# Performance work log

Measured on AMD Instinct MI355X. Metric: run time of the kernel, lower is better.

## Reference

```python
import jax, jax.numpy as jnp
import numpy as np
import math

B, S, D_IN, EMBED, H = 4, 1024, 1024, 1024, 16
HD = EMBED // H  # 64


def setup_inputs() -> dict:
    key = jax.random.key(0)
    ks = jax.random.split(key, 8)
    x = jax.random.normal(ks[0], (B, S, D_IN), dtype=jnp.float32)
    mask = jax.random.randint(ks[1], (B, S, S), 0, 2, dtype=jnp.int32)
    weights = jax.random.uniform(ks[2], (B, S, S), dtype=jnp.float32)
    # xavier-uniform-ish scale for projections
    lim_qkv = math.sqrt(6.0 / (D_IN + 3 * EMBED))
    lim_o = math.sqrt(6.0 / (EMBED + EMBED))
    W_qkv = jax.random.uniform(ks[3], (3 * EMBED, D_IN), minval=-lim_qkv, maxval=lim_qkv, dtype=jnp.float32)
    b_qkv = jnp.zeros((3 * EMBED,), dtype=jnp.float32)
    W_o = jax.random.uniform(ks[4], (EMBED, EMBED), minval=-lim_o, maxval=lim_o, dtype=jnp.float32)
    b_o = jnp.zeros((EMBED,), dtype=jnp.float32)
    return {"x": x, "mask": mask, "weights": weights, "W_qkv": W_qkv, "b_qkv": b_qkv, "W_o": W_o, "b_o": b_o}


def reference(x, mask, weights, W_qkv, b_qkv, W_o, b_o):
    b, s, _ = x.shape
    # QKV projection: [b, s, 3*EMBED] -> [b, H, s, 3*HD]
    qkv = (x @ W_qkv.T + b_qkv).reshape(b, s, H, 3 * HD).transpose(0, 2, 1, 3)
    q, k, v = jnp.split(qkv, 3, axis=-1)  # each [b, H, s, HD]
    logits = jnp.einsum('bhqd,bhkd->bhqk', q, k) / math.sqrt(HD)
    logits = jnp.where(mask[:, None, :, :] == 0, jnp.float32(-9e15), logits)
    # weights transposed on last two dims, broadcast over heads
    w = jnp.swapaxes(weights, -2, -1)[:, None, :, :]  # [b, 1, s, s]
    m = jnp.max(logits, axis=-1, keepdims=True)
    e = w * jnp.exp(logits - m)
    attn = e / jnp.sum(e, axis=-1, keepdims=True)
    vals = jnp.einsum('bhqk,bhkd->bhqd', attn, v)
    vals = vals.transpose(0, 2, 1, 3).reshape(b, s, EMBED)
    return vals @ W_o.T + b_o
```

## Files before the change

kernel.cpp:

```cpp
#include <hip/hip_runtime.h>
#include <hip/hip_bf16.h>
#include <stdint.h>

#define SDIM 1024
#define BATCH 4
#define NH 16
#define HDIM 64
#define KDIM 1024
#define N_QKV 3072
#define EMB 1024

typedef uint16_t u16;
typedef __attribute__((ext_vector_type(4))) float f32x4;
typedef __attribute__((ext_vector_type(8))) short bf16x8;
typedef __attribute__((ext_vector_type(8))) unsigned short u16x8;

__device__ __forceinline__ u16 f2bf(float f) {
  union { float f; uint32_t u; } x; x.f = f;
  uint32_t r = x.u + 0x7FFFu + ((x.u >> 16) & 1u);
  return (u16)(r >> 16);
}

__device__ __forceinline__ float bf2f(u16 b) {
  union { uint32_t u; float f; } x; x.u = ((uint32_t)b) << 16;
  return x.f;
}

__device__ __forceinline__ void gload_lds16(const u16* g, u16* l) {
  __builtin_amdgcn_global_load_lds(
      (const __attribute__((address_space(1))) unsigned int*)g,
      (__attribute__((address_space(3))) unsigned int*)l, 16, 0, 0);
}

#define N8_X  524288
#define N8_WQ 393216
#define N8_WO 131072
#define NCVT  1048576
#define NWM3  262144
__global__ void prep_kernel(const float* __restrict__ a, const float* __restrict__ bq,
                            const float* __restrict__ co,
                            u16* __restrict__ oa, u16* __restrict__ ob, u16* __restrict__ oc,
                            const int* __restrict__ mask, const float* __restrict__ wts,
                            u16* __restrict__ wm3) {
  const int total = NCVT + NWM3;
  const size_t SS = (size_t)SDIM * SDIM;
  int stride = gridDim.x * blockDim.x;
  for (int i = blockIdx.x * blockDim.x + threadIdx.x; i < total; i += stride) {
    if (i < NCVT) {
      const float* s; u16* d; int j;
      if (i < N8_X)             { s = a;  d = oa; j = i; }
      else if (i < N8_X + N8_WQ){ s = bq; d = ob; j = i - N8_X; }
      else                      { s = co; d = oc; j = i - N8_X - N8_WQ; }
      const float4* s4 = (const float4*)s + (size_t)j * 2;
      float4 u = s4[0], v = s4[1];
      u16x8 o;
      o[0] = f2bf(u.x); o[1] = f2bf(u.y); o[2] = f2bf(u.z); o[3] = f2bf(u.w);
      o[4] = f2bf(v.x); o[5] = f2bf(v.y); o[6] = f2bf(v.z); o[7] = f2bf(v.w);
      ((u16x8*)d)[j] = o;
    } else {
      int t = i - NCVT;
      int lane = t & 63, kt = (t >> 6) & 15, T = (t >> 10) & 63, b = t >> 16;
      int g2 = lane >> 4, c2 = lane & 15;
      int q = T * 16 + c2;
      const int* mrow = mask + (size_t)b * SS + (size_t)q * SDIM;
      const float* wcol = wts + (size_t)b * SS + q;
      u16* dst = wm3 + ((size_t)(b * 64 + T) * 16 + kt) * 1024 + lane * 16;
      #pragma unroll
      for (int hf = 0; hf < 2; ++hf) {
        int bk = kt * 64 + 8 * g2 + 32 * hf;
        int4 m0 = *(const int4*)(mrow + bk);
        int4 m1 = *(const int4*)(mrow + bk + 4);
        int mm[8] = {m0.x, m0.y, m0.z, m0.w, m1.x, m1.y, m1.z, m1.w};
        u16x8 o;
        #pragma unroll
        for (int e = 0; e < 8; ++e)
          o[e] = mm[e] ? f2bf(wcol[(size_t)(bk + e) * SDIM]) : (u16)0;
        *(u16x8*)(dst + hf * 8) = o;
      }
    }
  }
}

__global__ __launch_bounds__(512, 1) void gemm_qkv(
    const u16* __restrict__ A, const u16* __restrict__ Bm,
    const float* __restrict__ bias,
    u16* __restrict__ Qh, u16* __restrict__ Kh, u16* __restrict__ Vt)
{
  __shared__ char smem[114688];
  const int tid = threadIdx.x;
  const int gid = blockIdx.x;
  const int brow = (gid & 15) * 256, bcol = (gid >> 4) * 192;
  const int wid = tid >> 6, lane = tid & 63;
  const int g = lane >> 4, c = lane & 15, cx = c & 7;
  const int wr = wid & 3, wc = wid >> 2;

  const u16* asrc[4]; int adoff[4];
  #pragma unroll
  for (int j = 0; j < 4; ++j) {
    int i = j * 512 + tid;
    int row = i >> 3, sch = (i & 7) ^ (row & 7);
    asrc[j] = A + (size_t)(brow + row) * KDIM + sch * 8;
    adoff[j] = (j * 512 + wid * 64) * 16;
  }
  const u16* bsrc[3]; int bdoff[3];
  #pragma unroll
  for (int j = 0; j < 3; ++j) {
    int i = j * 512 + tid;
    int row = i >> 3, sch = (i & 7) ^ (row & 7);
    bsrc[j] = Bm + (size_t)(bcol + row) * KDIM + sch * 8;
    bdoff[j] = 32768 + (j * 512 + wid * 64) * 16;
  }

  auto stage = [&](int kt, int slot) {
    char* base = smem + slot * 57344;
    #pragma unroll
    for (int j = 0; j < 4; ++j)
      gload_lds16(asrc[j] + kt * 64, (u16*)(base + adoff[j]));
    #pragma unroll
    for (int j = 0; j < 3; ++j)
      gload_lds16(bsrc[j] + kt * 64, (u16*)(base + bdoff[j]));
  };

  f32x4 acc[4][6] = {};

  stage(0, 0);
  __syncthreads();

  for (int kt = 0; kt < 16; ++kt) {
    if (kt < 15) stage(kt + 1, (kt + 1) & 1);

    const char* As = smem + (kt & 1) * 57344;
    const char* Bs = As + 32768;

    #pragma unroll
    for (int kk = 0; kk < 2; ++kk) {
      bf16x8 af[4], bfr[6];
      #pragma unroll
      for (int m = 0; m < 4; ++m) {
        int row = wr * 64 + m * 16 + c;
        af[m] = *(const bf16x8*)(As + (row << 7) + ((((kk << 2) + g) ^ cx) << 4));
      }
      #pragma unroll
      for (int n = 0; n < 6; ++n) {
        int row = wc * 96 + n * 16 + c;
        bfr[n] = *(const bf16x8*)(Bs + (row << 7) + ((((kk << 2) + g) ^ cx) << 4));
      }
      __builtin_amdgcn_s_setprio(1);
      #pragma unroll
      for (int m = 0; m < 4; ++m)
        #pragma unroll
        for (int n = 0; n < 6; ++n)
          acc[m][n] = __builtin_amdgcn_mfma_f32_16x16x32_bf16(
              af[m], bfr[n], acc[m][n], 0, 0, 0);
      __builtin_amdgcn_s_setprio(0);
    }
    __syncthreads();
  }

  #pragma unroll
  for (int m = 0; m < 4; ++m) {
    #pragma unroll
    for (int n = 0; n < 6; ++n) {
      int col = bcol + wc * 96 + n * 16 + c;
      float bv = bias[col];
      int h = col / 192;
      int rem = col - h * 192;
      int sec = rem >> 6, d = rem & 63;
      #pragma unroll
      for (int r = 0; r < 4; ++r) {
        int row = brow + wr * 64 + m * 16 + g * 4 + r;
        int b = row >> 10, sl = row & 1023;
        float v = acc[m][n][r] + bv;
        if (sec == 0)
          Qh[((size_t)(b * NH + h) * SDIM + sl) * HDIM + d] = f2bf(v * 0.125f);
        else if (sec == 1)
          Kh[((size_t)(b * NH + h) * SDIM + sl) * HDIM + d] = f2bf(v);
        else
          Vt[((size_t)(b * NH + h) * HDIM + d) * SDIM + sl] = f2bf(v);
      }
    }
  }
}

__global__ __launch_bounds__(256) void gemm_bt(
    const u16* __restrict__ A, const u16* __restrict__ Bm,
    const float* __restrict__ bias, float* __restrict__ C,
    int M, int N, int K)
{
  __shared__ u16 As[128 * 64];
  __shared__ u16 Bs[128 * 64];
  const int tid = threadIdx.x;
  const int wid = tid >> 6, lane = tid & 63;
  const int g = lane >> 4, c = lane & 15, cx = c & 7;
  const int wrow = (wid >> 1) * 64, wcol = (wid & 1) * 64;
  const int brow = blockIdx.x * 128, bcol = blockIdx.y * 128;

  const u16* asrc[4]; const u16* bsrc[4]; u16* adst[4]; u16* bdst[4];
  #pragma unroll
  for (int j = 0; j < 4; ++j) {
    int ci = j * 256 + tid;
    int row = ci >> 3, sch = (ci & 7) ^ (row & 7);
    asrc[j] = A  + (size_t)(brow + row) * K + sch * 8;
    bsrc[j] = Bm + (size_t)(bcol + row) * K + sch * 8;
    adst[j] = As + (j * 256 + wid * 64) * 8;
    bdst[j] = Bs + (j * 256 + wid * 64) * 8;
  }

  f32x4 acc[4][4] = {};
  const char* Asc = (const char*)As;
  const char* Bsc = (const char*)Bs;

  for (int kt = 0; kt < K / 64; ++kt) {
    #pragma unroll
    for (int j = 0; j < 4; ++j) {
      gload_lds16(asrc[j] + kt * 64, adst[j]);
      gload_lds16(bsrc[j] + kt * 64, bdst[j]);
    }
    __syncthreads();

    bf16x8 af[2][4], bfr[2][4];
    #pragma unroll
    for (int kk = 0; kk < 2; ++kk)
      #pragma unroll
      for (int i = 0; i < 4; ++i) {
        int cha = ((kk << 2) + g) ^ cx;
        af[kk][i]  = *(const bf16x8*)(Asc + ((wrow + i * 16 + c) << 7) + (cha << 4));
        bfr[kk][i] = *(const bf16x8*)(Bsc + ((wcol + i * 16 + c) << 7) + (cha << 4));
      }
    #pragma unroll
    for (int kk = 0; kk < 2; ++kk)
      #pragma unroll
      for (int mi = 0; mi < 4; ++mi)
        #pragma unroll
        for (int ni = 0; ni < 4; ++ni)
          acc[mi][ni] = __builtin_amdgcn_mfma_f32_16x16x32_bf16(
              af[kk][mi], bfr[kk][ni], acc[mi][ni], 0, 0, 0);
    __syncthreads();
  }

  #pragma unroll
  for (int mi = 0; mi < 4; ++mi)
    #pragma unroll
    for (int ni = 0; ni < 4; ++ni) {
      int col = bcol + wcol + ni * 16 + c;
      float bv = bias[col];
      #pragma unroll
      for (int r = 0; r < 4; ++r) {
        int row = brow + wrow + mi * 16 + g * 4 + r;
        C[(size_t)row * N + col] = acc[mi][ni][r] + bv;
      }
    }
}

__global__ __launch_bounds__(256, 4) void attn_kernel(
    const u16* __restrict__ Qh, const u16* __restrict__ Kh, const u16* __restrict__ Vt,
    const u16* __restrict__ wm3, u16* __restrict__ vals)
{
  int bid = blockIdx.x;
  int swz = (bid & 7) * 128 + (bid >> 3);
  const int qt = swz & 15, bh = swz >> 4;
  const int h = bh & 15, b = bh >> 4;

  const int tid = threadIdx.x;
  const int wid = tid >> 6, lane = tid & 63;
  const int g = lane >> 4, c = lane & 15;
  const int qloc = qt * 64 + wid * 16;

  __shared__ u16 Kb[2][4096];
  __shared__ u16 Vb[2][4096];

  const u16* qp = Qh + ((size_t)bh * SDIM + qloc + c) * HDIM;
  bf16x8 qa0 = *(const bf16x8*)(qp + g * 8);
  bf16x8 qa1 = *(const bf16x8*)(qp + 32 + g * 8);

  const u16* kbase = Kh + (size_t)bh * SDIM * HDIM;
  const u16* vbase = Vt + (size_t)bh * HDIM * SDIM;
  const u16* wbase = wm3 + (((size_t)(b * 16 + qt) * 4 + wid) * 16) * 1024 + lane * 16;

  float l_run = 0.f;
  f32x4 acc_o[4] = {};

  auto fsw = [](int row) { return ((row ^ (row >> 3)) & 7) ^ ((row & 1) << 2); };

  int kro[4], kxr[4], vro[4], vxr[4];
  #pragma unroll
  for (int st = 0; st < 4; ++st) {
    int kr = ((c >> 2) << 3) + ((st & 1) << 2) + (c & 3) + ((st >> 1) << 5);
    kro[st] = kr << 7;
    kxr[st] = fsw(kr);
  }
  #pragma unroll
  for (int dt = 0; dt < 4; ++dt) {
    int vr = dt * 16 + c;
    vro[dt] = vr << 7;
    vxr[dt] = fsw(vr);
  }

  auto stage = [&](int buf, int kt) {
    const int k0 = kt * 64;
    #pragma unroll
    for (int j = 0; j < 2; ++j) {
      int i = j * 256 + tid;
      int row = i >> 3;
      int sch = (i & 7) ^ (((row ^ (row >> 3)) & 7) ^ ((row & 1) << 2));
      gload_lds16(kbase + (size_t)(k0 + row) * HDIM + sch * 8,
                  &Kb[buf][(size_t)(j * 256 + wid * 64) * 8]);
      gload_lds16(vbase + (size_t)row * SDIM + k0 + sch * 8,
                  &Vb[buf][(size_t)(j * 256 + wid * 64) * 8]);
    }
  };

  stage(0, 0);
  __syncthreads();
  int cur = 0;

  for (int kt = 0; kt < 16; ++kt) {
    if (kt < 15) stage(cur ^ 1, kt + 1);

    u16x8 w0 = *(const u16x8*)(wbase + kt * 1024);
    u16x8 w1 = *(const u16x8*)(wbase + kt * 1024 + 8);

    const char* kb = (const char*)&Kb[cur][0];
    const char* vb = (const char*)&Vb[cur][0];

    f32x4 sc[4];
    #pragma unroll
    for (int st = 0; st < 4; ++st) {
      bf16x8 ka0 = *(const bf16x8*)(kb + kro[st] + ((g ^ kxr[st]) << 4));
      bf16x8 ka1 = *(const bf16x8*)(kb + kro[st] + (((4 + g) ^ kxr[st]) << 4));
      f32x4 z = {};
      z = __builtin_amdgcn_mfma_f32_16x16x32_bf16(ka0, qa0, z, 0, 0, 0);
      z = __builtin_amdgcn_mfma_f32_16x16x32_bf16(ka1, qa1, z, 0, 0, 0);
      sc[st] = z;
    }

    float p[4][4];
    #pragma unroll
    for (int st = 0; st < 4; ++st) {
      #pragma unroll
      for (int r = 0; r < 4; ++r) {
        u16 wv = (st < 2) ? ((const u16*)&w0)[st * 4 + r]
                          : ((const u16*)&w1)[(st - 2) * 4 + r];
        float pv = bf2f(wv) * __expf(sc[st][r]);
        p[st][r] = pv;
        l_run += pv;
      }
    }

    uint32_t pk[8];
    #pragma unroll
    for (int i = 0; i < 8; ++i) {
      float lo = p[i >> 1][(i & 1) * 2], hi = p[i >> 1][(i & 1) * 2 + 1];
      asm("v_cvt_pk_bf16_f32 %0, %1, %2" : "=v"(pk[i]) : "v"(lo), "v"(hi));
    }
    union PA { uint32_t u[4]; bf16x8 v; } a0, a1;
    #pragma unroll
    for (int i = 0; i < 4; ++i) { a0.u[i] = pk[i]; a1.u[i] = pk[4 + i]; }

    #pragma unroll
    for (int dt = 0; dt < 4; ++dt) {
      bf16x8 vb0 = *(const bf16x8*)(vb + vro[dt] + ((g ^ vxr[dt]) << 4));
      bf16x8 vb1 = *(const bf16x8*)(vb + vro[dt] + (((4 + g) ^ vxr[dt]) << 4));
      acc_o[dt] = __builtin_amdgcn_mfma_f32_16x16x32_bf16(a0.v, vb0, acc_o[dt], 0, 0, 0);
      acc_o[dt] = __builtin_amdgcn_mfma_f32_16x16x32_bf16(a1.v, vb1, acc_o[dt], 0, 0, 0);
    }

    __syncthreads();
    cur ^= 1;
  }

  l_run += __shfl_xor(l_run, 16);
  l_run += __shfl_xor(l_run, 32);

  float inv[4];
  #pragma unroll
  for (int r = 0; r < 4; ++r)
    inv[r] = 1.0f / __shfl(l_run, g * 4 + r);

  #pragma unroll
  for (int dt = 0; dt < 4; ++dt)
    #pragma unroll
    for (int r = 0; r < 4; ++r) {
      int row = b * SDIM + qloc + g * 4 + r;
      vals[(size_t)row * EMB + h * HDIM + dt * 16 + c] = f2bf(acc_o[dt][r] * inv[r]);
    }
}

extern "C" void kernel_launch(void* const* d_in, const int* in_sizes, int n_in,
                              void* d_out, int out_size, void* d_ws, size_t ws_size,
                              hipStream_t stream) {
  const float* x     = (const float*)d_in[0];
  const int*   mask  = (const int*)d_in[1];
  const float* wts   = (const float*)d_in[2];
  const float* W_qkv = (const float*)d_in[3];
  const float* b_qkv = (const float*)d_in[4];
  const float* W_o   = (const float*)d_in[5];
  const float* b_o   = (const float*)d_in[6];
  float* out = (float*)d_out;

  char* ws = (char*)d_ws;
  u16* xb   = (u16*)(ws);
  u16* wqb  = (u16*)(ws + (8ull  << 20));
  u16* wob  = (u16*)(ws + (14ull << 20));
  u16* Qh   = (u16*)(ws + (16ull << 20));
  u16* Kh   = (u16*)(ws + (24ull << 20));
  u16* Vt   = (u16*)(ws + (32ull << 20));
  u16* valb = (u16*)(ws + (40ull << 20));
  u16* wm3b = (u16*)d_out;

  prep_kernel<<<2048, 256, 0, stream>>>(x, W_qkv, W_o, xb, wqb, wob, mask, wts, wm3b);

  gemm_qkv<<<256, 512, 0, stream>>>(xb, wqb, b_qkv, Qh, Kh, Vt);

  attn_kernel<<<1024, 256, 0, stream>>>(Qh, Kh, Vt, wm3b, valb);

  dim3 g3(32, 8);
  gemm_bt<<<g3, 256, 0, stream>>>(valb, wob, b_o, out, BATCH * SDIM, EMB, KDIM);
}
```

Before: 108.9 us.

## Restructure QKV GEMM into 256x256 tiles with fine-grained interleaved staging pipeline

The QKV projection GEMM moves from 256x192 tiles on 256 blocks to 256x256 tiles on 192 blocks, using a 2x4 warp layout in which each warp holds 128x64 of the output. The main loop is now hand-scheduled: global-to-LDS loads for the next tiles are issued in half-tile chunks between MFMA quarters, synchronized with explicit s_barrier, waitcnt and sched_barrier. The goal is to overlap memory traffic with matrix math and raise arithmetic intensity per block. The cost is 128KB of LDS per block, so launch_bounds(512,2) probably cannot actually fit two blocks per CU, and 192 blocks leave some of the 256 CUs idle.

```diff
diff --git a/kernel.cpp b/kernel.cpp
--- a/kernel.cpp
+++ b/kernel.cpp
@@ -81,94 +81,154 @@
   }
 }
 
-__global__ __launch_bounds__(512, 1) void gemm_qkv(
+__global__ __launch_bounds__(512, 2) void gemm_qkv(
     const u16* __restrict__ A, const u16* __restrict__ Bm,
     const float* __restrict__ bias,
     u16* __restrict__ Qh, u16* __restrict__ Kh, u16* __restrict__ Vt)
 {
-  __shared__ char smem[114688];
+  __shared__ char smem[131072];
   const int tid = threadIdx.x;
   const int gid = blockIdx.x;
-  const int brow = (gid & 15) * 256, bcol = (gid >> 4) * 192;
+  const int brow = (gid & 15) * 256, bcol = (gid >> 4) * 256;
   const int wid = tid >> 6, lane = tid & 63;
   const int g = lane >> 4, c = lane & 15, cx = c & 7;
-  const int wr = wid & 3, wc = wid >> 2;
-
-  const u16* asrc[4]; int adoff[4];
-  #pragma unroll
-  for (int j = 0; j < 4; ++j) {
-    int i = j * 512 + tid;
-    int row = i >> 3, sch = (i & 7) ^ (row & 7);
-    asrc[j] = A + (size_t)(brow + row) * KDIM + sch * 8;
-    adoff[j] = (j * 512 + wid * 64) * 16;
-  }
-  const u16* bsrc[3]; int bdoff[3];
-  #pragma unroll
-  for (int j = 0; j < 3; ++j) {
-    int i = j * 512 + tid;
-    int row = i >> 3, sch = (i & 7) ^ (row & 7);
-    bsrc[j] = Bm + (size_t)(bcol + row) * KDIM + sch * 8;
-    bdoff[j] = 32768 + (j * 512 + wid * 64) * 16;
-  }
-
-  auto stage = [&](int kt, int slot) {
-    char* base = smem + slot * 57344;
-    #pragma unroll
-    for (int j = 0; j < 4; ++j)
-      gload_lds16(asrc[j] + kt * 64, (u16*)(base + adoff[j]));
-    #pragma unroll
-    for (int j = 0; j < 3; ++j)
-      gload_lds16(bsrc[j] + kt * 64, (u16*)(base + bdoff[j]));
+  const int wr = wid >> 2, wc = wid & 3;
+
+  int srow[2], ssch[2], sdst[2];
+  #pragma unroll
+  for (int j = 0; j < 2; ++j) {
+    int ci = j * 512 + tid;
+    srow[j] = ci >> 3;
+    ssch[j] = (ci & 7) ^ (srow[j] & 7);
+    sdst[j] = (j * 512 + wid * 64) * 16;
+  }
+
+  auto stageA = [&](int half, int kt, int db) {
+    #pragma unroll
+    for (int j = 0; j < 2; ++j)
+      gload_lds16(A + (size_t)(brow + half * 128 + srow[j]) * KDIM + kt * 64 + ssch[j] * 8,
+                  (u16*)(smem + db * 65536 + half * 16384 + sdst[j]));
   };
-
-  f32x4 acc[4][6] = {};
-
-  stage(0, 0);
-  __syncthreads();
-
-  for (int kt = 0; kt < 16; ++kt) {
-    if (kt < 15) stage(kt + 1, (kt + 1) & 1);
-
-    const char* As = smem + (kt & 1) * 57344;
-    const char* Bs = As + 32768;
-
-    #pragma unroll
-    for (int kk = 0; kk < 2; ++kk) {
-      bf16x8 af[4], bfr[6];
-      #pragma unroll
-      for (int m = 0; m < 4; ++m) {
-        int row = wr * 64 + m * 16 + c;
-        af[m] = *(const bf16x8*)(As + (row << 7) + ((((kk << 2) + g) ^ cx) << 4));
-      }
-      #pragma unroll
-      for (int n = 0; n < 6; ++n) {
-        int row = wc * 96 + n * 16 + c;
-        bfr[n] = *(const bf16x8*)(Bs + (row << 7) + ((((kk << 2) + g) ^ cx) << 4));
-      }
-      __builtin_amdgcn_s_setprio(1);
-      #pragma unroll
-      for (int m = 0; m < 4; ++m)
-        #pragma unroll
-        for (int n = 0; n < 6; ++n)
-          acc[m][n] = __builtin_amdgcn_mfma_f32_16x16x32_bf16(
-              af[m], bfr[n], acc[m][n], 0, 0, 0);
-      __builtin_amdgcn_s_setprio(0);
-    }
-    __syncthreads();
-  }
-
-  #pragma unroll
-  for (int m = 0; m < 4; ++m) {
-    #pragma unroll
-    for (int n = 0; n < 6; ++n) {
-      int col = bcol + wc * 96 + n * 16 + c;
+  auto stageB = [&](int half, int kt, int db) {
+    #pragma unroll
+    for (int j = 0; j < 2; ++j)
+      gload_lds16(Bm + (size_t)(bcol + half * 128 + srow[j]) * KDIM + kt * 64 + ssch[j] * 8,
+                  (u16*)(smem + db * 65536 + 32768 + half * 16384 + sdst[j]));
+  };
+
+  auto ldsA = [&](int db, int m, int kk) {
+    return *(const bf16x8*)(smem + db * 65536 + wr * 16384 +
+                            ((m * 16 + c) << 7) + ((((kk << 2) + g) ^ cx) << 4));
+  };
+  auto ldsB = [&](int db, int n, int kk) {
+    return *(const bf16x8*)(smem + db * 65536 + 32768 + (wc >> 1) * 16384 +
+                            (((wc & 1) * 64 + n * 16 + c) << 7) + ((((kk << 2) + g) ^ cx) << 4));
+  };
+
+  f32x4 acc[8][4] = {};
+  bf16x8 af[4][2], bfr[4][2];
+
+#define BARRIER()  asm volatile("s_barrier" ::: "memory")
+#define LGKM0()    asm volatile("s_waitcnt lgkmcnt(0)" ::: "memory")
+#define VMC2()     asm volatile("s_waitcnt vmcnt(2)" ::: "memory")
+#define SCHED0()   __builtin_amdgcn_sched_barrier(0)
+#define MFMA_Q(MB, NB)                                                     \
+  __builtin_amdgcn_s_setprio(1);                                           \
+  _Pragma("unroll") for (int kk = 0; kk < 2; ++kk)                         \
+  _Pragma("unroll") for (int m = 0; m < 4; ++m)                            \
+  _Pragma("unroll") for (int n = 0; n < 2; ++n)                            \
+    acc[MB + m][NB + n] = __builtin_amdgcn_mfma_f32_16x16x32_bf16(         \
+        af[m][kk], bfr[NB + n][kk], acc[MB + m][NB + n], 0, 0, 0);         \
+  __builtin_amdgcn_s_setprio(0)
+
+  stageA(0, 0, 0); stageA(1, 0, 0); stageB(0, 0, 0); stageB(1, 0, 0);
+  stageA(0, 1, 1);
+  VMC2();
+  BARRIER();
+  SCHED0();
+
+  for (int it = 0; it < 8; ++it) {
+    const int t1 = 2 * it + 1;
+    int t2 = 2 * it + 2; if (t2 > 15) t2 -= 2;
+    int t3 = 2 * it + 3; if (t3 > 15) t3 -= 2;
+
+    #pragma unroll
+    for (int m = 0; m < 4; ++m) { af[m][0] = ldsA(0, m, 0); af[m][1] = ldsA(0, m, 1); }
+    #pragma unroll
+    for (int n = 0; n < 2; ++n) { bfr[n][0] = ldsB(0, n, 0); bfr[n][1] = ldsB(0, n, 1); }
+    stageA(1, t1, 1);
+    BARRIER(); LGKM0(); SCHED0();
+    MFMA_Q(0, 0);
+    BARRIER(); SCHED0();
+
+    #pragma unroll
+    for (int n = 2; n < 4; ++n) { bfr[n][0] = ldsB(0, n, 0); bfr[n][1] = ldsB(0, n, 1); }
+    stageB(0, t1, 1);
+    BARRIER(); LGKM0(); SCHED0();
+    MFMA_Q(0, 2);
+    BARRIER(); SCHED0();
+
+    #pragma unroll
+    for (int m = 0; m < 4; ++m) { af[m][0] = ldsA(0, m + 4, 0); af[m][1] = ldsA(0, m + 4, 1); }
+    stageB(1, t1, 1);
+    BARRIER(); LGKM0(); SCHED0();
+    MFMA_Q(4, 0);
+    BARRIER(); SCHED0();
+
+    stageA(0, t2, 0);
+    BARRIER(); SCHED0();
+    MFMA_Q(4, 2);
+    VMC2();
+    BARRIER(); SCHED0();
+
+    #pragma unroll
+    for (int m = 0; m < 4; ++m) { af[m][0] = ldsA(1, m, 0); af[m][1] = ldsA(1, m, 1); }
+    #pragma unroll
+    for (int n = 0; n < 2; ++n) { bfr[n][0] = ldsB(1, n, 0); bfr[n][1] = ldsB(1, n, 1); }
+    stageA(1, t2, 0);
+    BARRIER(); LGKM0(); SCHED0();
+    MFMA_Q(0, 0);
+    BARRIER(); SCHED0();
+
+    #pragma unroll
+    for (int n = 2; n < 4; ++n) { bfr[n][0] = ldsB(1, n, 0); bfr[n][1] = ldsB(1, n, 1); }
+    stageB(0, t2, 0);
+    BARRIER(); LGKM0(); SCHED0();
+    MFMA_Q(0, 2);
+    BARRIER(); SCHED0();
+
+    #pragma unroll
+    for (int m = 0; m < 4; ++m) { af[m][0] = ldsA(1, m + 4, 0); af[m][1] = ldsA(1, m + 4, 1); }
+    stageB(1, t2, 0);
+    BARRIER(); LGKM0(); SCHED0();
+    MFMA_Q(4, 0);
+    BARRIER(); SCHED0();
+
+    stageA(0, t3, 1);
+    BARRIER(); SCHED0();
+    MFMA_Q(4, 2);
+    VMC2();
+    BARRIER(); SCHED0();
+  }
+
+#undef BARRIER
+#undef LGKM0
+#undef VMC2
+#undef SCHED0
+#undef MFMA_Q
+
+  #pragma unroll
+  for (int m = 0; m < 8; ++m) {
+    #pragma unroll
+    for (int n = 0; n < 4; ++n) {
+      int col = bcol + wc * 64 + n * 16 + c;
       float bv = bias[col];
       int h = col / 192;
       int rem = col - h * 192;
       int sec = rem >> 6, d = rem & 63;
       #pragma unroll
       for (int r = 0; r < 4; ++r) {
-        int row = brow + wr * 64 + m * 16 + g * 4 + r;
+        int row = brow + wr * 128 + m * 16 + g * 4 + r;
         int b = row >> 10, sl = row & 1023;
         float v = acc[m][n][r] + bv;
         if (sec == 0)
@@ -410,7 +470,7 @@
 
   prep_kernel<<<2048, 256, 0, stream>>>(x, W_qkv, W_o, xb, wqb, wob, mask, wts, wm3b);
 
-  gemm_qkv<<<256, 512, 0, stream>>>(xb, wqb, b_qkv, Qh, Kh, Vt);
+  gemm_qkv<<<192, 512, 0, stream>>>(xb, wqb, b_qkv, Qh, Kh, Vt);
 
   attn_kernel<<<1024, 256, 0, stream>>>(Qh, Kh, Vt, wm3b, valb);
 
```

Measured after the change: 120.3 us. 1.1x slower.
